# Performance work log

Measured on AMD Instinct MI355X. Metric: run time of the kernel, lower is better.

The kernel has to match this reference:

```python
import jax, jax.numpy as jnp
import numpy as np

NEG_SLOPE = 0.2
EPS = 1e-16


def add_self_loops(edge_index, num_nodes):
    loops = jnp.arange(num_nodes, dtype=edge_index.dtype)
    return jnp.concatenate([edge_index, jnp.stack([loops, loops])], axis=1)


def gat_conv(x, edge_index, W, att_src, att_dst, bias, concat):
    # PyG GATConv: linear -> per-head attention logits -> segment softmax over
    # incoming edges of each destination node -> weighted scatter-add.
    N = x.shape[0]
    H, C = att_src.shape
    ei = add_self_loops(edge_index, N)
    src, dst = ei[0], ei[1]
    h = (x @ W).reshape(N, H, C)                      # [N,H,C]
    a_src = jnp.einsum('nhc,hc->nh', h, att_src)       # [N,H]
    a_dst = jnp.einsum('nhc,hc->nh', h, att_dst)       # [N,H]
    logits = jax.nn.leaky_relu(a_src[src] + a_dst[dst], NEG_SLOPE)  # [E,H]
    m = jax.ops.segment_max(logits, dst, num_segments=N)            # [N,H]
    e = jnp.exp(logits - m[dst])
    s = jax.ops.segment_sum(e, dst, num_segments=N)                 # [N,H]
    alpha = e / (s[dst] + EPS)                                      # [E,H]
    out = jax.ops.segment_sum(h[src] * alpha[:, :, None], dst, num_segments=N)  # [N,H,C]
    out = out.reshape(N, H * C) if concat else out.mean(axis=1)
    return out + bias


def setup_inputs() -> dict:
    key = jax.random.key(0)
    ks = jax.random.split(key, 10)
    N, E, F_in, Hd, heads, F_out = 50000, 800000, 128, 32, 4, 64
    return {
        'x': jax.random.normal(ks[0], (N, F_in), jnp.float32),
        'edge_index': jax.random.randint(ks[1], (2, E), 0, N, jnp.int64),
        'W1': jax.random.normal(ks[2], (F_in, heads * Hd), jnp.float32) * 0.1,
        'att_src1': jax.random.normal(ks[3], (heads, Hd), jnp.float32) * 0.1,
        'att_dst1': jax.random.normal(ks[4], (heads, Hd), jnp.float32) * 0.1,
        'bias1': jax.random.normal(ks[5], (heads * Hd,), jnp.float32) * 0.1,
        'W2': jax.random.normal(ks[6], (heads * Hd, heads * F_out), jnp.float32) * 0.1,
        'att_src2': jax.random.normal(ks[7], (heads, F_out), jnp.float32) * 0.1,
        'att_dst2': jax.random.normal(ks[8], (heads, F_out), jnp.float32) * 0.1,
        'bias2': jax.random.normal(ks[9], (F_out,), jnp.float32) * 0.1,
    }


def reference(x, edge_index, W1, att_src1, att_dst1, bias1, W2, att_src2, att_dst2, bias2):
    h = gat_conv(x, edge_index, W1, att_src1, att_dst1, bias1, concat=True)
    h = jax.nn.elu(h)  # dropout p=0.0 / eval mode -> identity
    out = gat_conv(h, edge_index, W2, att_src2, att_dst2, bias2, concat=False)
    return out
```

## Files before the change

kernel.cpp:

```cpp
#include <hip/hip_runtime.h>

typedef unsigned int uint;
typedef unsigned short ushort;


__device__ __forceinline__ float leaky(float x) { return x >= 0.f ? x : 0.2f * x; }
__device__ __forceinline__ float b2f(ushort h) { return __uint_as_float(((uint)h) << 16); }
__device__ __forceinline__ ushort f2b(float f) {
    uint u = __float_as_uint(f);
    return (ushort)((u + 0x7FFF + ((u >> 16) & 1)) >> 16);
}

#if defined(__has_builtin)
#if __has_builtin(__builtin_amdgcn_fdot2_f32_bf16)
#define HAS_DOT2 1
#endif
#endif
#ifndef HAS_DOT2
#define HAS_DOT2 0
#endif

#if HAS_DOT2
typedef __bf16 bf16v2 __attribute__((ext_vector_type(2)));
__device__ __forceinline__ float dot2bf(uint h2, uint w2, float c) {
    return __builtin_amdgcn_fdot2_f32_bf16(__builtin_bit_cast(bf16v2, h2),
                                           __builtin_bit_cast(bf16v2, w2), c, false);
}
#define DOT2PAIR(hE, hE1, wpk, a0, a1)                                  \
    a0 = dot2bf(__builtin_amdgcn_perm(hE, hE1, 0x01000504), wpk, a0);   \
    a1 = dot2bf(__builtin_amdgcn_perm(hE, hE1, 0x03020706), wpk, a1);
#else
#define DOT2PAIR(hE, hE1, wpk, a0, a1)                                  \
    {                                                                   \
        float wlo = __uint_as_float((wpk) << 16);                       \
        float whi = __uint_as_float((wpk) & 0xffff0000u);               \
        a0 = fmaf(wlo, __uint_as_float((hE) << 16), a0);                \
        a1 = fmaf(wlo, __uint_as_float((hE) & 0xffff0000u), a1);        \
        a0 = fmaf(whi, __uint_as_float((hE1) << 16), a0);               \
        a1 = fmaf(whi, __uint_as_float((hE1) & 0xffff0000u), a1);       \
    }
#endif

__device__ __forceinline__ int detect_bf_local(const void* xin) {
    __shared__ int s_sane;
    if (threadIdx.x == 0) s_sane = 0;
    __syncthreads();
    ushort v = ((const ushort*)xin)[2 * threadIdx.x];
    int ex = (v >> 7) & 0xFF;
    if (v == 0 || (ex >= 100 && ex <= 135)) atomicAdd(&s_sane, 1);
    __syncthreads();
    return s_sane >= 230;
}
__device__ __forceinline__ int detect_is64_local(const int* ei) {
    __shared__ int s_odd;
    if (threadIdx.x == 0) s_odd = 0;
    __syncthreads();
    if (threadIdx.x < 64 && ei[2 * threadIdx.x + 1] != 0) atomicOr(&s_odd, 1);
    __syncthreads();
    return s_odd == 0;
}

__device__ __forceinline__ float rdf(const void* p_, int i, int bf) {
    return bf ? b2f(((const ushort*)p_)[i]) : ((const float*)p_)[i];
}

__device__ __forceinline__ int edge_dst(const int* __restrict__ ei, int E, int e, int is64) {
    return (e >= E) ? (e - E) : (is64 ? ei[2 * E + 2 * e] : ei[E + e]);
}

__global__ void prep_kernel(const void* __restrict__ x, const void* __restrict__ W1,
                            const void* __restrict__ as1, const void* __restrict__ ad1,
                            const void* __restrict__ b1, const void* __restrict__ b2,
                            const void* __restrict__ W2, const void* __restrict__ as2,
                            const void* __restrict__ ad2, const int* __restrict__ ei,
                            int E, int ET,
                            ushort* __restrict__ W1T, float* __restrict__ att1,
                            float* __restrict__ b1f, float* __restrict__ b2f_,
                            float* __restrict__ w2t8, ushort* __restrict__ W2sT,
                            int* __restrict__ flagI, int* __restrict__ flagF,
                            int* __restrict__ bcnt) {
    int b = blockIdx.x, t = threadIdx.x;
    if (b < 64) {
        int bf = detect_bf_local(x);
        int i = b * 256 + t;
        int k = i >> 7, n = i & 127;
        W1T[n * 128 + k] = bf ? ((const ushort*)W1)[i] : f2b(((const float*)W1)[i]);
        return;
    }
    b -= 64;
    if (b == 0) {
        int bf = detect_bf_local(x);
        int is64 = detect_is64_local(ei);
        if (t == 0) { *flagF = bf; *flagI = is64; }
        for (int i = t; i < 512; i += 256) {
            if (i < 128)      att1[i] = rdf(as1, i, bf);
            else if (i < 256) att1[i] = rdf(ad1, i - 128, bf);
            else if (i < 384) b1f[i - 256] = rdf(b1, i - 256, bf);
            else if (i < 448) b2f_[i - 384] = rdf(b2, i - 384, bf);
        }
        return;
    }
    b -= 1;
    if (b < 4) {
        int bf = detect_bf_local(x);
        int idx = b * 256 + t;
        int o = idx >> 7, k = idx & 127, h = o & 3;
        const void* att = (o < 4) ? as2 : ad2;
        float s = 0.f;
        for (int c = 0; c < 64; ++c) s += rdf(W2, k * 256 + h * 64 + c, bf) * rdf(att, h * 64 + c, bf);
        w2t8[o * 128 + k] = s;
        return;
    }
    b -= 4;
    if (b < 128) {
        int bf = detect_bf_local(x);
        int idx = b * 256 + t;
        int c = idx >> 9, hk = idx & 511;
        int h = hk >> 7, k = hk & 127;
        W2sT[c * 512 + hk] = f2b(0.25f * rdf(W2, k * 256 + h * 64 + c, bf));
        return;
    }
    b -= 128;
    {
        int is64 = detect_is64_local(ei);
        __shared__ int bins[256];
        bins[t] = 0;
        __syncthreads();
        int base = b * 4096;
        for (int i = 0; i < 16; ++i) {
            int e = base + i * 256 + t;
            if (e < ET) atomicAdd(&bins[edge_dst(ei, E, e, is64) >> 8], 1);
        }
        __syncthreads();
        if (bins[t]) atomicAdd(&bcnt[t], bins[t]);
    }
}

__global__ __launch_bounds__(256) void bscan_kernel(const int* __restrict__ bcnt,
                                                    int* __restrict__ bbase,
                                                    int* __restrict__ gcur, int NBUK) {
    __shared__ int sc[256];
    int t = threadIdx.x;
    int v = (t < NBUK) ? bcnt[t] : 0;
    sc[t] = v;
    __syncthreads();
    for (int off = 1; off < 256; off <<= 1) {
        int a = (t >= off) ? sc[t - off] : 0;
        __syncthreads();
        sc[t] += a;
        __syncthreads();
    }
    int excl = sc[t] - v;
    if (t < NBUK) { bbase[t] = excl; gcur[t] = excl; }
    if (t == 255) bbase[NBUK] = sc[255];
}

__global__ __launch_bounds__(256) void part_kernel(const int* __restrict__ ei, int E, int ET,
                                                   const int* __restrict__ flagI,
                                                   int* __restrict__ gcur,
                                                   uint* __restrict__ ebuf, int NBUK) {
    __shared__ uint stage[8192];
    __shared__ int cnt_s[256], sc[256], lbase[257], cur[256], gb[256];
    int t = threadIdx.x;
    int base = blockIdx.x * 8192;
    cnt_s[t] = 0;
    __syncthreads();
    int is64 = *flagI;
    uint pk[32];
    short bk[32];
#pragma unroll
    for (int i = 0; i < 32; ++i) {
        int e = base + i * 256 + t;
        if (e < ET) {
            int src, dst;
            if (e >= E) { src = dst = e - E; }
            else if (is64) { src = ei[2 * e]; dst = ei[2 * E + 2 * e]; }
            else           { src = ei[e];     dst = ei[E + e]; }
            pk[i] = (uint)src | ((uint)dst << 16);
            bk[i] = (short)(dst >> 8);
            atomicAdd(&cnt_s[bk[i]], 1);
        } else bk[i] = -1;
    }
    __syncthreads();
    int v = cnt_s[t];
    sc[t] = v;
    __syncthreads();
    for (int off = 1; off < 256; off <<= 1) {
        int a = (t >= off) ? sc[t - off] : 0;
        __syncthreads();
        sc[t] += a;
        __syncthreads();
    }
    lbase[t + 1] = sc[t];
    cur[t] = sc[t] - v;
    if (t == 0) lbase[0] = 0;
    __syncthreads();
#pragma unroll
    for (int i = 0; i < 32; ++i)
        if (bk[i] >= 0) {
            int slot = atomicAdd(&cur[bk[i]], 1);
            stage[slot] = pk[i];
        }
    __syncthreads();
    if (t < NBUK) {
        int c = lbase[t + 1] - lbase[t];
        if (c > 0) gb[t] = atomicAdd(&gcur[t], c);
    }
    __syncthreads();
    int total = lbase[256];
    for (int i = t; i < total; i += 256) {
        int lo = 0, hi = 255;
        while (lo < hi) { int mid = (lo + hi + 1) >> 1; if (lbase[mid] <= i) lo = mid; else hi = mid - 1; }
        ebuf[gb[lo] + (i - lbase[lo])] = stage[i];
    }
}

__global__ __launch_bounds__(256) void bfinal_kernel(const uint* __restrict__ ebuf,
                                                     const int* __restrict__ bbase,
                                                     int* __restrict__ rowptr,
                                                     int* __restrict__ ecol, int N, int NBUK) {
    __shared__ int hist[2048], cur2[2048], ws[4];
    int b = blockIdx.x, t = threadIdx.x;
    int lane = t & 63, wid = t >> 6;
    int d0 = b << 8;
#pragma unroll
    for (int j = 0; j < 8; ++j) hist[t * 8 + j] = 0;
    __syncthreads();
    int s = bbase[b], e2 = bbase[b + 1];
    for (int i = s + t; i < e2; i += 256) {
        uint pk = ebuf[i];
        int key = (((int)(pk >> 16) - d0) << 3) | (int)((pk & 0xffffu) >> 13);
        atomicAdd(&hist[key], 1);
    }
    __syncthreads();
    int loc[8];
    int v = 0;
#pragma unroll
    for (int j = 0; j < 8; ++j) { loc[j] = v; v += hist[t * 8 + j]; }
    int incl = v;
#pragma unroll
    for (int off = 1; off < 64; off <<= 1) {
        int a = __shfl_up(incl, off, 64);
        if (lane >= off) incl += a;
    }
    if (lane == 63) ws[wid] = incl;
    __syncthreads();
    if (t == 0) {
        int acc = 0;
        for (int j = 0; j < 4; ++j) { int x = ws[j]; ws[j] = acc; acc += x; }
    }
    __syncthreads();
    int excl = incl - v + ws[wid];
    int d = d0 + t;
    if (d < N) rowptr[d] = s + excl;
#pragma unroll
    for (int j = 0; j < 8; ++j) cur2[t * 8 + j] = s + excl + loc[j];
    if (b == NBUK - 1 && t == 0) rowptr[N] = bbase[NBUK];
    __syncthreads();
    for (int i = s + t; i < e2; i += 256) {
        uint pk = ebuf[i];
        int key = (((int)(pk >> 16) - d0) << 3) | (int)((pk & 0xffffu) >> 13);
        int pos = atomicAdd(&cur2[key], 1);
        ecol[pos] = (int)(pk & 0xffffu);
    }
}

__global__ void hist_kernel(const int* __restrict__ ei, int E, int N,
                            const int* __restrict__ flag, int* __restrict__ deg) {
    int e = blockIdx.x * blockDim.x + threadIdx.x;
    if (e >= E + N) return;
    atomicAdd(&deg[edge_dst(ei, E, e, *flag)], 1);
}
__global__ void scatter_kernel(const int* __restrict__ ei, int E, int N,
                               const int* __restrict__ flag, const int* __restrict__ rowptr,
                               int* __restrict__ cnt, int* __restrict__ ecol) {
    int e = blockIdx.x * blockDim.x + threadIdx.x;
    if (e >= E + N) return;
    int src, dst;
    if (e >= E) { src = dst = e - E; }
    else if (*flag) { src = ei[2 * e]; dst = ei[2 * E + 2 * e]; }
    else            { src = ei[e];     dst = ei[E + e]; }
    int pos = rowptr[dst] + atomicAdd(&cnt[dst], 1);
    ecol[pos] = src;
}
__global__ __launch_bounds__(1024) void scan1_kernel(const int* __restrict__ deg,
                                                     int* __restrict__ tmp,
                                                     int* __restrict__ bsum, int n) {
    __shared__ int ws[16];
    int tid = threadIdx.x, lane = tid & 63, wid = tid >> 6;
    int i = blockIdx.x * 1024 + tid;
    int v = (i < n) ? deg[i] : 0;
    int incl = v;
#pragma unroll
    for (int off = 1; off < 64; off <<= 1) {
        int t2 = __shfl_up(incl, off, 64);
        if (lane >= off) incl += t2;
    }
    if (lane == 63) ws[wid] = incl;
    __syncthreads();
    if (tid < 16) {
        int wv_ = ws[tid], winc = wv_;
#pragma unroll
        for (int off = 1; off < 16; off <<= 1) {
            int t2 = __shfl_up(winc, off, 16);
            if (tid >= off) winc += t2;
        }
        ws[tid] = winc - wv_;
    }
    __syncthreads();
    int excl = incl - v + ws[wid];
    if (i < n) tmp[i] = excl;
    if (tid == 1023) bsum[blockIdx.x] = excl + v;
}
__global__ void scan2_kernel(int* __restrict__ bsum, int nb) {
    int lane = threadIdx.x;
    int v = (lane < nb) ? bsum[lane] : 0;
    int incl = v;
    for (int off = 1; off < 64; off <<= 1) {
        int t = __shfl_up(incl, off, 64);
        if (lane >= off) incl += t;
    }
    int total = __shfl(incl, nb - 1, 64);
    if (lane < nb) bsum[lane] = incl - v;
    if (lane == 0) bsum[nb] = total;
}
__global__ void scan3_kernel(const int* __restrict__ tmp, const int* __restrict__ bsum,
                             int* __restrict__ rowptr, int* __restrict__ cnt, int n, int nb) {
    int i = blockIdx.x * blockDim.x + threadIdx.x;
    if (i > n) return;
    rowptr[i] = (i == n) ? bsum[nb] : tmp[i] + bsum[i >> 10];
    if (i < n) cnt[i] = 0;
}

typedef __attribute__((ext_vector_type(8))) short bf16x8;
typedef __attribute__((ext_vector_type(4))) float floatx4;

__global__ __launch_bounds__(256) void gemm1_kernel(
    const void* __restrict__ xraw, const int* __restrict__ flagF,
    const ushort* __restrict__ BT, ushort* __restrict__ C,
    const float* __restrict__ att, float4* __restrict__ asrc4, float4* __restrict__ adst4, int M) {
    constexpr int K = 128, NT = 8;
    int lane = threadIdx.x & 63, wv = threadIdx.x >> 6;
    int row0 = (blockIdx.x * 4 + wv) * 16;
    if (row0 >= M) return;
    int m = lane & 15, quad = lane >> 4;
    int rowa = min(row0 + m, M - 1);
    bf16x8 af[4];
    if (*flagF) {
        const bf16x8* arow = (const bf16x8*)((const ushort*)xraw + (size_t)rowa * K);
#pragma unroll
        for (int kk = 0; kk < 4; ++kk) af[kk] = arow[4 * kk + quad];
    } else {
        const float4* arw = (const float4*)((const float*)xraw + (size_t)rowa * K);
#pragma unroll
        for (int kk = 0; kk < 4; ++kk) {
            float4 fa = arw[2 * (4 * kk + quad)];
            float4 fb = arw[2 * (4 * kk + quad) + 1];
            bf16x8 tv;
            tv[0] = (short)f2b(fa.x); tv[1] = (short)f2b(fa.y);
            tv[2] = (short)f2b(fa.z); tv[3] = (short)f2b(fa.w);
            tv[4] = (short)f2b(fb.x); tv[5] = (short)f2b(fb.y);
            tv[6] = (short)f2b(fb.z); tv[7] = (short)f2b(fb.w);
            af[kk] = tv;
        }
    }
    floatx4 acc[NT] = {};
#pragma unroll
    for (int nt = 0; nt < NT; ++nt) {
        const bf16x8* brow = (const bf16x8*)(BT + (size_t)(nt * 16 + m) * K);
#pragma unroll
        for (int kk = 0; kk < 4; ++kk)
            acc[nt] = __builtin_amdgcn_mfma_f32_16x16x32_bf16(af[kk], brow[4 * kk + quad], acc[nt], 0, 0, 0);
    }
#pragma unroll
    for (int nt = 0; nt < NT; ++nt)
#pragma unroll
        for (int r = 0; r < 4; ++r) {
            int row = row0 + quad * 4 + r;
            if (row < M) C[(size_t)row * 128 + nt * 16 + m] = f2b(acc[nt][r]);
        }
    float attS[NT], attD[NT];
#pragma unroll
    for (int nt = 0; nt < NT; ++nt) { attS[nt] = att[nt * 16 + m]; attD[nt] = att[128 + nt * 16 + m]; }
#pragma unroll
    for (int r = 0; r < 4; ++r) {
        float ps[4] = {0, 0, 0, 0}, pd[4] = {0, 0, 0, 0};
#pragma unroll
        for (int nt = 0; nt < NT; ++nt) {
            int h = nt / 2;
            ps[h] = fmaf(acc[nt][r], attS[nt], ps[h]);
            pd[h] = fmaf(acc[nt][r], attD[nt], pd[h]);
        }
#pragma unroll
        for (int off = 1; off < 16; off <<= 1) {
#pragma unroll
            for (int h = 0; h < 4; ++h) {
                ps[h] += __shfl_xor(ps[h], off, 64);
                pd[h] += __shfl_xor(pd[h], off, 64);
            }
        }
        int row = row0 + quad * 4 + r;
        if (m == 0 && row < M) {
            asrc4[row] = make_float4(ps[0], ps[1], ps[2], ps[3]);
            adst4[row] = make_float4(pd[0], pd[1], pd[2], pd[3]);
        }
    }
}

__global__ __launch_bounds__(256) void agg1_kernel(
    const ushort* __restrict__ hsrc, const float4* __restrict__ a_src4,
    const float4* __restrict__ a_dst4, const int* __restrict__ rowptr,
    const int* __restrict__ ecol, const float* __restrict__ bias,
    const float* __restrict__ w2t8, uint4* __restrict__ outz,
    float4* __restrict__ asrc2, float4* __restrict__ adst2, int N) {
    constexpr int SH = 7;
    __shared__ __align__(16) ushort elds[4][4][4][20];
    int lane = threadIdx.x & 63, wv = threadIdx.x >> 6;
    int q = lane >> 4, c = lane & 15, qbase = q << 4;
    int n = blockIdx.x * 16 + wv * 4 + q;
    bool nv = n < N;
    int start = 0, end = 0;
    if (nv) { start = rowptr[n]; end = rowptr[n + 1]; }
    int deg = end - start;
    float4 ad = nv ? a_dst4[n] : make_float4(0.f, 0.f, 0.f, 0.f);
    int hh = c >> 2;
    uint laneoff = (uint)c * 8;
    float acc[8] = {};
    float ss0 = 0.f, ss1 = 0.f, ss2 = 0.f, ss3 = 0.f;

    for (int cs = 0; cs < deg; cs += 16) {
        int len = min(16, deg - cs);
        bool v = c < len;
        int sv = v ? ecol[start + cs + c] : 0;
        float4 as = a_src4[sv];
        float e0 = v ? __expf(fminf(leaky(as.x + ad.x), 60.f)) : 0.f;
        float e1 = v ? __expf(fminf(leaky(as.y + ad.y), 60.f)) : 0.f;
        float e2 = v ? __expf(fminf(leaky(as.z + ad.z), 60.f)) : 0.f;
        float e3 = v ? __expf(fminf(leaky(as.w + ad.w), 60.f)) : 0.f;
        ushort r0 = f2b(e0), r1 = f2b(e1), r2 = f2b(e2), r3 = f2b(e3);
        elds[wv][0][q][c] = r0; elds[wv][1][q][c] = r1;
        elds[wv][2][q][c] = r2; elds[wv][3][q][c] = r3;
        ss0 += b2f(r0); ss1 += b2f(r1); ss2 += b2f(r2); ss3 += b2f(r3);
        for (int e = 0; e < len; e += 4) {
            int s0 = __shfl(sv, qbase + e + 0, 64);
            int s1 = __shfl(sv, qbase + e + 1, 64);
            int s2 = __shfl(sv, qbase + e + 2, 64);
            int s3 = __shfl(sv, qbase + e + 3, 64);
            uint2 w = *(const uint2*)&elds[wv][hh][q][e];
            uint4 h0 = *(const uint4*)(hsrc + (((uint)s0) << SH) + laneoff);
            uint4 h1 = *(const uint4*)(hsrc + (((uint)s1) << SH) + laneoff);
            uint4 h2 = *(const uint4*)(hsrc + (((uint)s2) << SH) + laneoff);
            uint4 h3 = *(const uint4*)(hsrc + (((uint)s3) << SH) + laneoff);
            DOT2PAIR(h0.x, h1.x, w.x, acc[0], acc[1]); DOT2PAIR(h0.y, h1.y, w.x, acc[2], acc[3]);
            DOT2PAIR(h0.z, h1.z, w.x, acc[4], acc[5]); DOT2PAIR(h0.w, h1.w, w.x, acc[6], acc[7]);
            DOT2PAIR(h2.x, h3.x, w.y, acc[0], acc[1]); DOT2PAIR(h2.y, h3.y, w.y, acc[2], acc[3]);
            DOT2PAIR(h2.z, h3.z, w.y, acc[4], acc[5]); DOT2PAIR(h2.w, h3.w, w.y, acc[6], acc[7]);
        }
    }
#pragma unroll
    for (int off = 1; off < 16; off <<= 1) {
        ss0 += __shfl_xor(ss0, off, 64); ss1 += __shfl_xor(ss1, off, 64);
        ss2 += __shfl_xor(ss2, off, 64); ss3 += __shfl_xor(ss3, off, 64);
    }
    if (!nv) return;
    float ih = (hh == 0) ? 1.f / (ss0 + 1e-16f) : (hh == 1) ? 1.f / (ss1 + 1e-16f)
             : (hh == 2) ? 1.f / (ss2 + 1e-16f) : 1.f / (ss3 + 1e-16f);
    float4 bA = ((const float4*)bias)[2 * c], bB = ((const float4*)bias)[2 * c + 1];
    float o[8];
    o[0] = acc[0] * ih + bA.x; o[1] = acc[1] * ih + bA.y;
    o[2] = acc[2] * ih + bA.z; o[3] = acc[3] * ih + bA.w;
    o[4] = acc[4] * ih + bB.x; o[5] = acc[5] * ih + bB.y;
    o[6] = acc[6] * ih + bB.z; o[7] = acc[7] * ih + bB.w;
#pragma unroll
    for (int j = 0; j < 8; ++j) o[j] = o[j] > 0.f ? o[j] : __expf(o[j]) - 1.f;
    uint4 pk;
    pk.x = (uint)f2b(o[0]) | ((uint)f2b(o[1]) << 16);
    pk.y = (uint)f2b(o[2]) | ((uint)f2b(o[3]) << 16);
    pk.z = (uint)f2b(o[4]) | ((uint)f2b(o[5]) << 16);
    pk.w = (uint)f2b(o[6]) | ((uint)f2b(o[7]) << 16);
    outz[(size_t)n * 16 + c] = pk;

    float po[8];
#pragma unroll
    for (int oo = 0; oo < 8; ++oo) {
        float4 wA = ((const float4*)(w2t8 + oo * 128))[2 * c];
        float4 wB = ((const float4*)(w2t8 + oo * 128))[2 * c + 1];
        po[oo] = o[0] * wA.x + o[1] * wA.y + o[2] * wA.z + o[3] * wA.w
               + o[4] * wB.x + o[5] * wB.y + o[6] * wB.z + o[7] * wB.w;
    }
#pragma unroll
    for (int off = 1; off < 16; off <<= 1)
#pragma unroll
        for (int oo = 0; oo < 8; ++oo) po[oo] += __shfl_xor(po[oo], off, 64);
    if (c == 0) {
        asrc2[n] = make_float4(po[0], po[1], po[2], po[3]);
        adst2[n] = make_float4(po[4], po[5], po[6], po[7]);
    }
}

__global__ __launch_bounds__(256) void agg2_kernel(
    const ushort* __restrict__ hsrc, const float4* __restrict__ a_src4,
    const float4* __restrict__ a_dst4, const int* __restrict__ rowptr,
    const int* __restrict__ ecol, const ushort* __restrict__ W2sT,
    const float* __restrict__ b2, float* __restrict__ outp, int N) {
    constexpr int SH = 7;
    __shared__ __align__(16) ushort elds[4][4][4][20];
    __shared__ __align__(16) ushort lds_a[16][520];
    int lane = threadIdx.x & 63, wv = threadIdx.x >> 6;
    int q = lane >> 4, c = lane & 15, qbase = q << 4;
    int n = blockIdx.x * 16 + wv * 4 + q;
    bool nv = n < N;
    int start = 0, end = 0;
    if (nv) { start = rowptr[n]; end = rowptr[n + 1]; }
    int deg = end - start;
    float4 ad = nv ? a_dst4[n] : make_float4(0.f, 0.f, 0.f, 0.f);
    uint laneoff = (uint)c * 8;
    float a0_[8] = {}, a1_[8] = {}, a2_[8] = {}, a3_[8] = {};
    float ss0 = 0.f, ss1 = 0.f, ss2 = 0.f, ss3 = 0.f;

    for (int cs = 0; cs < deg; cs += 16) {
        int len = min(16, deg - cs);
        bool v = c < len;
        int sv = v ? ecol[start + cs + c] : 0;
        float4 as = a_src4[sv];
        float e0 = v ? __expf(fminf(leaky(as.x + ad.x), 60.f)) : 0.f;
        float e1 = v ? __expf(fminf(leaky(as.y + ad.y), 60.f)) : 0.f;
        float e2 = v ? __expf(fminf(leaky(as.z + ad.z), 60.f)) : 0.f;
        float e3 = v ? __expf(fminf(leaky(as.w + ad.w), 60.f)) : 0.f;
        ushort r0 = f2b(e0), r1 = f2b(e1), r2 = f2b(e2), r3 = f2b(e3);
        elds[wv][0][q][c] = r0; elds[wv][1][q][c] = r1;
        elds[wv][2][q][c] = r2; elds[wv][3][q][c] = r3;
        ss0 += b2f(r0); ss1 += b2f(r1); ss2 += b2f(r2); ss3 += b2f(r3);
        for (int e = 0; e < len; e += 4) {
            int s0 = __shfl(sv, qbase + e + 0, 64);
            int s1 = __shfl(sv, qbase + e + 1, 64);
            int s2 = __shfl(sv, qbase + e + 2, 64);
            int s3 = __shfl(sv, qbase + e + 3, 64);
            uint2 w0 = *(const uint2*)&elds[wv][0][q][e];
            uint2 w1 = *(const uint2*)&elds[wv][1][q][e];
            uint2 w2 = *(const uint2*)&elds[wv][2][q][e];
            uint2 w3 = *(const uint2*)&elds[wv][3][q][e];
            uint4 h0 = *(const uint4*)(hsrc + (((uint)s0) << SH) + laneoff);
            uint4 h1 = *(const uint4*)(hsrc + (((uint)s1) << SH) + laneoff);
            uint4 h2 = *(const uint4*)(hsrc + (((uint)s2) << SH) + laneoff);
            uint4 h3 = *(const uint4*)(hsrc + (((uint)s3) << SH) + laneoff);
            DOT2PAIR(h0.x, h1.x, w0.x, a0_[0], a0_[1]); DOT2PAIR(h0.y, h1.y, w0.x, a0_[2], a0_[3]);
            DOT2PAIR(h0.z, h1.z, w0.x, a0_[4], a0_[5]); DOT2PAIR(h0.w, h1.w, w0.x, a0_[6], a0_[7]);
            DOT2PAIR(h0.x, h1.x, w1.x, a1_[0], a1_[1]); DOT2PAIR(h0.y, h1.y, w1.x, a1_[2], a1_[3]);
            DOT2PAIR(h0.z, h1.z, w1.x, a1_[4], a1_[5]); DOT2PAIR(h0.w, h1.w, w1.x, a1_[6], a1_[7]);
            DOT2PAIR(h0.x, h1.x, w2.x, a2_[0], a2_[1]); DOT2PAIR(h0.y, h1.y, w2.x, a2_[2], a2_[3]);
            DOT2PAIR(h0.z, h1.z, w2.x, a2_[4], a2_[5]); DOT2PAIR(h0.w, h1.w, w2.x, a2_[6], a2_[7]);
            DOT2PAIR(h0.x, h1.x, w3.x, a3_[0], a3_[1]); DOT2PAIR(h0.y, h1.y, w3.x, a3_[2], a3_[3]);
            DOT2PAIR(h0.z, h1.z, w3.x, a3_[4], a3_[5]); DOT2PAIR(h0.w, h1.w, w3.x, a3_[6], a3_[7]);
            DOT2PAIR(h2.x, h3.x, w0.y, a0_[0], a0_[1]); DOT2PAIR(h2.y, h3.y, w0.y, a0_[2], a0_[3]);
            DOT2PAIR(h2.z, h3.z, w0.y, a0_[4], a0_[5]); DOT2PAIR(h2.w, h3.w, w0.y, a0_[6], a0_[7]);
            DOT2PAIR(h2.x, h3.x, w1.y, a1_[0], a1_[1]); DOT2PAIR(h2.y, h3.y, w1.y, a1_[2], a1_[3]);
            DOT2PAIR(h2.z, h3.z, w1.y, a1_[4], a1_[5]); DOT2PAIR(h2.w, h3.w, w1.y, a1_[6], a1_[7]);
            DOT2PAIR(h2.x, h3.x, w2.y, a2_[0], a2_[1]); DOT2PAIR(h2.y, h3.y, w2.y, a2_[2], a2_[3]);
            DOT2PAIR(h2.z, h3.z, w2.y, a2_[4], a2_[5]); DOT2PAIR(h2.w, h3.w, w2.y, a2_[6], a2_[7]);
            DOT2PAIR(h2.x, h3.x, w3.y, a3_[0], a3_[1]); DOT2PAIR(h2.y, h3.y, w3.y, a3_[2], a3_[3]);
            DOT2PAIR(h2.z, h3.z, w3.y, a3_[4], a3_[5]); DOT2PAIR(h2.w, h3.w, w3.y, a3_[6], a3_[7]);
        }
    }
#pragma unroll
    for (int off = 1; off < 16; off <<= 1) {
        ss0 += __shfl_xor(ss0, off, 64); ss1 += __shfl_xor(ss1, off, 64);
        ss2 += __shfl_xor(ss2, off, 64); ss3 += __shfl_xor(ss3, off, 64);
    }
    float i0 = 1.f / (ss0 + 1e-16f), i1 = 1.f / (ss1 + 1e-16f);
    float i2 = 1.f / (ss2 + 1e-16f), i3 = 1.f / (ss3 + 1e-16f);
    int slot = wv * 4 + q;
    uint4 pk;
    pk.x = (uint)f2b(a0_[0] * i0) | ((uint)f2b(a0_[1] * i0) << 16);
    pk.y = (uint)f2b(a0_[2] * i0) | ((uint)f2b(a0_[3] * i0) << 16);
    pk.z = (uint)f2b(a0_[4] * i0) | ((uint)f2b(a0_[5] * i0) << 16);
    pk.w = (uint)f2b(a0_[6] * i0) | ((uint)f2b(a0_[7] * i0) << 16);
    *(uint4*)&lds_a[slot][0 * 128 + 8 * c] = pk;
    pk.x = (uint)f2b(a1_[0] * i1) | ((uint)f2b(a1_[1] * i1) << 16);
    pk.y = (uint)f2b(a1_[2] * i1) | ((uint)f2b(a1_[3] * i1) << 16);
    pk.z = (uint)f2b(a1_[4] * i1) | ((uint)f2b(a1_[5] * i1) << 16);
    pk.w = (uint)f2b(a1_[6] * i1) | ((uint)f2b(a1_[7] * i1) << 16);
    *(uint4*)&lds_a[slot][1 * 128 + 8 * c] = pk;
    pk.x = (uint)f2b(a2_[0] * i2) | ((uint)f2b(a2_[1] * i2) << 16);
    pk.y = (uint)f2b(a2_[2] * i2) | ((uint)f2b(a2_[3] * i2) << 16);
    pk.z = (uint)f2b(a2_[4] * i2) | ((uint)f2b(a2_[5] * i2) << 16);
    pk.w = (uint)f2b(a2_[6] * i2) | ((uint)f2b(a2_[7] * i2) << 16);
    *(uint4*)&lds_a[slot][2 * 128 + 8 * c] = pk;
    pk.x = (uint)f2b(a3_[0] * i3) | ((uint)f2b(a3_[1] * i3) << 16);
    pk.y = (uint)f2b(a3_[2] * i3) | ((uint)f2b(a3_[3] * i3) << 16);
    pk.z = (uint)f2b(a3_[4] * i3) | ((uint)f2b(a3_[5] * i3) << 16);
    pk.w = (uint)f2b(a3_[6] * i3) | ((uint)f2b(a3_[7] * i3) << 16);
    *(uint4*)&lds_a[slot][3 * 128 + 8 * c] = pk;
    __syncthreads();

    int m = lane & 15, quad = lane >> 4;
    const bf16x8* arow = (const bf16x8*)&lds_a[m][0];
    const bf16x8* brow = (const bf16x8*)(W2sT + (size_t)(wv * 16 + m) * 512);
    floatx4 acc2 = {};
#pragma unroll
    for (int kk = 0; kk < 16; ++kk)
        acc2 = __builtin_amdgcn_mfma_f32_16x16x32_bf16(arow[4 * kk + quad], brow[4 * kk + quad], acc2, 0, 0, 0);
    float bb = b2[wv * 16 + m];
#pragma unroll
    for (int r = 0; r < 4; ++r) {
        int row = quad * 4 + r;
        int node = blockIdx.x * 16 + row;
        if (node < N) outp[(size_t)node * 64 + wv * 16 + m] = acc2[r] + bb;
    }
}

extern "C" void kernel_launch(void* const* d_in, const int* in_sizes, int n_in,
                              void* d_out, int out_size, void* d_ws, size_t ws_size,
                              hipStream_t stream) {
    const void* x_raw = d_in[0];
    const int*  ei    = (const int*)d_in[1];
    const void* W1_p  = d_in[2];
    const void* as1_p = d_in[3];
    const void* ad1_p = d_in[4];
    const void* b1_p  = d_in[5];
    const void* W2_p  = d_in[6];
    const void* as2_p = d_in[7];
    const void* ad2_p = d_in[8];
    const void* b2_p  = d_in[9];

    const int F_IN = 128;
    const int N = in_sizes[0] / F_IN;
    const int E = in_sizes[1] / 2;
    const int ET = E + N;
    const int NB = (N + 1023) / 1024;
    const int NBUK = (N + 255) >> 8;
    const int NBH = (ET + 4095) / 4096;

    char* p = (char*)d_ws;
    auto alloc = [&](size_t bytes) { char* r = p; p += (bytes + 255) & ~(size_t)255; return r; };
    ushort* W1T   = (ushort*)alloc(128 * 128 * 2);
    ushort* W2sT  = (ushort*)alloc(64 * 512 * 2);
    float*  att1f = (float*)alloc(256 * 4);
    float*  w2t8  = (float*)alloc(8 * 128 * 4);
    float*  b1f   = (float*)alloc(128 * 4);
    float*  b2f   = (float*)alloc(64 * 4);
    ushort* h1    = (ushort*)alloc((size_t)N * 128 * 2);
    ushort* hL1   = (ushort*)alloc((size_t)N * 128 * 2);
    float*  asrc1 = (float*)alloc((size_t)N * 4 * 4);
    float*  adst1 = (float*)alloc((size_t)N * 4 * 4);
    float*  asrc2 = (float*)alloc((size_t)N * 4 * 4);
    float*  adst2 = (float*)alloc((size_t)N * 4 * 4);
    int* deg    = (int*)alloc((size_t)N * 4);
    int* cnt    = (int*)alloc((size_t)N * 4);
    int* tmp    = (int*)alloc((size_t)N * 4);
    int* bsum   = (int*)alloc(128 * 4);
    int* rowptr = (int*)alloc((size_t)(N + 1) * 4);
    int* ecol   = (int*)alloc((size_t)ET * 4);
    uint* ebuf  = (uint*)alloc((size_t)ET * 4);
    int* bcnt   = (int*)alloc(256 * 4);
    int* bbase  = (int*)alloc(257 * 4);
    int* gcur   = (int*)alloc(256 * 4);
    int* flagI  = (int*)alloc(256);
    int* flagF  = (int*)alloc(256);

    hipMemsetAsync(bcnt, 0, 256 * 4, stream);
    prep_kernel<<<64 + 1 + 4 + 128 + NBH, 256, 0, stream>>>(
        x_raw, W1_p, as1_p, ad1_p, b1_p, b2_p, W2_p, as2_p, ad2_p, ei, E, ET,
        W1T, att1f, b1f, b2f, w2t8, W2sT, flagI, flagF, bcnt);

    if (N <= 65536) {
        bscan_kernel<<<1, 256, 0, stream>>>(bcnt, bbase, gcur, NBUK);
        part_kernel<<<(ET + 8191) / 8192, 256, 0, stream>>>(ei, E, ET, flagI, gcur, ebuf, NBUK);
        bfinal_kernel<<<NBUK, 256, 0, stream>>>(ebuf, bbase, rowptr, ecol, N, NBUK);
    } else {
        hipMemsetAsync(deg, 0, (size_t)N * 4, stream);
        int eblocks = (ET + 255) / 256;
        hist_kernel<<<eblocks, 256, 0, stream>>>(ei, E, N, flagI, deg);
        scan1_kernel<<<NB, 1024, 0, stream>>>(deg, tmp, bsum, N);
        scan2_kernel<<<1, 64, 0, stream>>>(bsum, NB);
        scan3_kernel<<<(N + 256) / 256, 256, 0, stream>>>(tmp, bsum, rowptr, cnt, N, NB);
        scatter_kernel<<<eblocks, 256, 0, stream>>>(ei, E, N, flagI, rowptr, cnt, ecol);
    }

    int nblocks16 = (N + 15) / 16;
    int gblocks = (N + 63) / 64;
    gemm1_kernel<<<gblocks, 256, 0, stream>>>(
        x_raw, flagF, W1T, h1, att1f, (float4*)asrc1, (float4*)adst1, N);
    agg1_kernel<<<nblocks16, 256, 0, stream>>>(
        h1, (const float4*)asrc1, (const float4*)adst1, rowptr, ecol, b1f, w2t8,
        (uint4*)hL1, (float4*)asrc2, (float4*)adst2, N);
    agg2_kernel<<<nblocks16, 256, 0, stream>>>(
        hL1, (const float4*)asrc2, (const float4*)adst2, rowptr, ecol, W2sT, b2f,
        (float*)d_out, N);
}
```

Before: 194.6 us.

## Fuse bucket scan into partition kernel and co-launch GEMM1 blocks with partitioning

```diff
diff --git a/kernel.cpp b/kernel.cpp
--- a/kernel.cpp
+++ b/kernel.cpp
@@ -136,31 +136,95 @@
     }
 }
 
-__global__ __launch_bounds__(256) void bscan_kernel(const int* __restrict__ bcnt,
-                                                    int* __restrict__ bbase,
-                                                    int* __restrict__ gcur, int NBUK) {
-    __shared__ int sc[256];
-    int t = threadIdx.x;
-    int v = (t < NBUK) ? bcnt[t] : 0;
-    sc[t] = v;
-    __syncthreads();
-    for (int off = 1; off < 256; off <<= 1) {
-        int a = (t >= off) ? sc[t - off] : 0;
-        __syncthreads();
-        sc[t] += a;
-        __syncthreads();
-    }
-    int excl = sc[t] - v;
-    if (t < NBUK) { bbase[t] = excl; gcur[t] = excl; }
-    if (t == 255) bbase[NBUK] = sc[255];
-}
-
-__global__ __launch_bounds__(256) void part_kernel(const int* __restrict__ ei, int E, int ET,
-                                                   const int* __restrict__ flagI,
-                                                   int* __restrict__ gcur,
-                                                   uint* __restrict__ ebuf, int NBUK) {
+typedef __attribute__((ext_vector_type(8))) short bf16x8;
+typedef __attribute__((ext_vector_type(4))) float floatx4;
+
+__device__ __forceinline__ void gemm1_body(
+    int blk, const void* __restrict__ xraw, const int* __restrict__ flagF,
+    const ushort* __restrict__ BT, ushort* __restrict__ C,
+    const float* __restrict__ att, float4* __restrict__ asrc4, float4* __restrict__ adst4,
+    int M) {
+    constexpr int K = 128, NT = 8;
+    int lane = threadIdx.x & 63, wv = threadIdx.x >> 6;
+    int row0 = (blk * 4 + wv) * 16;
+    if (row0 >= M) return;
+    int m = lane & 15, quad = lane >> 4;
+    int rowa = min(row0 + m, M - 1);
+    bf16x8 af[4];
+    if (*flagF) {
+        const bf16x8* arow = (const bf16x8*)((const ushort*)xraw + (size_t)rowa * K);
+#pragma unroll
+        for (int kk = 0; kk < 4; ++kk) af[kk] = arow[4 * kk + quad];
+    } else {
+        const float4* arw = (const float4*)((const float*)xraw + (size_t)rowa * K);
+#pragma unroll
+        for (int kk = 0; kk < 4; ++kk) {
+            float4 fa = arw[2 * (4 * kk + quad)];
+            float4 fb = arw[2 * (4 * kk + quad) + 1];
+            bf16x8 tv;
+            tv[0] = (short)f2b(fa.x); tv[1] = (short)f2b(fa.y);
+            tv[2] = (short)f2b(fa.z); tv[3] = (short)f2b(fa.w);
+            tv[4] = (short)f2b(fb.x); tv[5] = (short)f2b(fb.y);
+            tv[6] = (short)f2b(fb.z); tv[7] = (short)f2b(fb.w);
+            af[kk] = tv;
+        }
+    }
+    floatx4 acc[NT] = {};
+#pragma unroll
+    for (int nt = 0; nt < NT; ++nt) {
+        const bf16x8* brow = (const bf16x8*)(BT + (size_t)(nt * 16 + m) * K);
+#pragma unroll
+        for (int kk = 0; kk < 4; ++kk)
+            acc[nt] = __builtin_amdgcn_mfma_f32_16x16x32_bf16(af[kk], brow[4 * kk + quad], acc[nt], 0, 0, 0);
+    }
+#pragma unroll
+    for (int nt = 0; nt < NT; ++nt)
+#pragma unroll
+        for (int r = 0; r < 4; ++r) {
+            int row = row0 + quad * 4 + r;
+            if (row < M) C[(size_t)row * 128 + nt * 16 + m] = f2b(acc[nt][r]);
+        }
+    float attS[NT], attD[NT];
+#pragma unroll
+    for (int nt = 0; nt < NT; ++nt) { attS[nt] = att[nt * 16 + m]; attD[nt] = att[128 + nt * 16 + m]; }
+#pragma unroll
+    for (int r = 0; r < 4; ++r) {
+        float ps[4] = {0, 0, 0, 0}, pd[4] = {0, 0, 0, 0};
+#pragma unroll
+        for (int nt = 0; nt < NT; ++nt) {
+            int h = nt / 2;
+            ps[h] = fmaf(acc[nt][r], attS[nt], ps[h]);
+            pd[h] = fmaf(acc[nt][r], attD[nt], pd[h]);
+        }
+#pragma unroll
+        for (int off = 1; off < 16; off <<= 1) {
+#pragma unroll
+            for (int h = 0; h < 4; ++h) {
+                ps[h] += __shfl_xor(ps[h], off, 64);
+                pd[h] += __shfl_xor(pd[h], off, 64);
+            }
+        }
+        int row = row0 + quad * 4 + r;
+        if (m == 0 && row < M) {
+            asrc4[row] = make_float4(ps[0], ps[1], ps[2], ps[3]);
+            adst4[row] = make_float4(pd[0], pd[1], pd[2], pd[3]);
+        }
+    }
+}
+
+__global__ __launch_bounds__(256) void partg_kernel(
+    const int* __restrict__ ei, int E, int ET, const int* __restrict__ flagI,
+    const int* __restrict__ bcnt, int* __restrict__ gofs, uint* __restrict__ ebuf,
+    int NBUK, int npart,
+    const void* __restrict__ xraw, const int* __restrict__ flagF,
+    const ushort* __restrict__ BT, ushort* __restrict__ C, const float* __restrict__ att,
+    float4* __restrict__ asrc4, float4* __restrict__ adst4, int M) {
+    if ((int)blockIdx.x >= npart) {
+        gemm1_body(blockIdx.x - npart, xraw, flagF, BT, C, att, asrc4, adst4, M);
+        return;
+    }
     __shared__ uint stage[8192];
-    __shared__ int cnt_s[256], sc[256], lbase[257], cur[256], gb[256];
+    __shared__ int cnt_s[256], sc[256], sc2[256], lbase[257], cur[256], gb[256];
     int t = threadIdx.x;
     int base = blockIdx.x * 8192;
     cnt_s[t] = 0;
@@ -183,16 +247,20 @@
     }
     __syncthreads();
     int v = cnt_s[t];
+    int v2 = (t < NBUK) ? bcnt[t] : 0;
     sc[t] = v;
+    sc2[t] = v2;
     __syncthreads();
     for (int off = 1; off < 256; off <<= 1) {
-        int a = (t >= off) ? sc[t - off] : 0;
+        int a  = (t >= off) ? sc[t - off]  : 0;
+        int a2 = (t >= off) ? sc2[t - off] : 0;
         __syncthreads();
-        sc[t] += a;
+        sc[t] += a; sc2[t] += a2;
         __syncthreads();
     }
     lbase[t + 1] = sc[t];
     cur[t] = sc[t] - v;
+    int bbx = sc2[t] - v2;
     if (t == 0) lbase[0] = 0;
     __syncthreads();
 #pragma unroll
@@ -204,7 +272,7 @@
     __syncthreads();
     if (t < NBUK) {
         int c = lbase[t + 1] - lbase[t];
-        if (c > 0) gb[t] = atomicAdd(&gcur[t], c);
+        if (c > 0) gb[t] = bbx + atomicAdd(&gofs[t], c);
     }
     __syncthreads();
     int total = lbase[256];
@@ -216,17 +284,26 @@
 }
 
 __global__ __launch_bounds__(256) void bfinal_kernel(const uint* __restrict__ ebuf,
-                                                     const int* __restrict__ bbase,
+                                                     const int* __restrict__ bcnt,
                                                      int* __restrict__ rowptr,
                                                      int* __restrict__ ecol, int N, int NBUK) {
-    __shared__ int hist[2048], cur2[2048], ws[4];
+    __shared__ int hist[2048], cur2[2048], ws[4], bb[256];
     int b = blockIdx.x, t = threadIdx.x;
     int lane = t & 63, wid = t >> 6;
     int d0 = b << 8;
+    bb[t] = (t < NBUK) ? bcnt[t] : 0;
 #pragma unroll
     for (int j = 0; j < 8; ++j) hist[t * 8 + j] = 0;
     __syncthreads();
-    int s = bbase[b], e2 = bbase[b + 1];
+    for (int off = 1; off < 256; off <<= 1) {
+        int a = (t >= off) ? bb[t - off] : 0;
+        __syncthreads();
+        bb[t] += a;
+        __syncthreads();
+    }
+    int s = (b == 0) ? 0 : bb[b - 1];
+    int e2 = bb[b];
+    int total = bb[255];
     for (int i = s + t; i < e2; i += 256) {
         uint pk = ebuf[i];
         int key = (((int)(pk >> 16) - d0) << 3) | (int)((pk & 0xffffu) >> 13);
@@ -255,7 +332,7 @@
     if (d < N) rowptr[d] = s + excl;
 #pragma unroll
     for (int j = 0; j < 8; ++j) cur2[t * 8 + j] = s + excl + loc[j];
-    if (b == NBUK - 1 && t == 0) rowptr[N] = bbase[NBUK];
+    if (b == NBUK - 1 && t == 0) rowptr[N] = total;
     __syncthreads();
     for (int i = s + t; i < e2; i += 256) {
         uint pk = ebuf[i];
@@ -332,79 +409,11 @@
     if (i < n) cnt[i] = 0;
 }
 
-typedef __attribute__((ext_vector_type(8))) short bf16x8;
-typedef __attribute__((ext_vector_type(4))) float floatx4;
-
 __global__ __launch_bounds__(256) void gemm1_kernel(
     const void* __restrict__ xraw, const int* __restrict__ flagF,
     const ushort* __restrict__ BT, ushort* __restrict__ C,
     const float* __restrict__ att, float4* __restrict__ asrc4, float4* __restrict__ adst4, int M) {
-    constexpr int K = 128, NT = 8;
-    int lane = threadIdx.x & 63, wv = threadIdx.x >> 6;
-    int row0 = (blockIdx.x * 4 + wv) * 16;
-    if (row0 >= M) return;
-    int m = lane & 15, quad = lane >> 4;
-    int rowa = min(row0 + m, M - 1);
-    bf16x8 af[4];
-    if (*flagF) {
-        const bf16x8* arow = (const bf16x8*)((const ushort*)xraw + (size_t)rowa * K);
-#pragma unroll
-        for (int kk = 0; kk < 4; ++kk) af[kk] = arow[4 * kk + quad];
-    } else {
-        const float4* arw = (const float4*)((const float*)xraw + (size_t)rowa * K);
-#pragma unroll
-        for (int kk = 0; kk < 4; ++kk) {
-            float4 fa = arw[2 * (4 * kk + quad)];
-            float4 fb = arw[2 * (4 * kk + quad) + 1];
-            bf16x8 tv;
-            tv[0] = (short)f2b(fa.x); tv[1] = (short)f2b(fa.y);
-            tv[2] = (short)f2b(fa.z); tv[3] = (short)f2b(fa.w);
-            tv[4] = (short)f2b(fb.x); tv[5] = (short)f2b(fb.y);
-            tv[6] = (short)f2b(fb.z); tv[7] = (short)f2b(fb.w);
-            af[kk] = tv;
-        }
-    }
-    floatx4 acc[NT] = {};
-#pragma unroll
-    for (int nt = 0; nt < NT; ++nt) {
-        const bf16x8* brow = (const bf16x8*)(BT + (size_t)(nt * 16 + m) * K);
-#pragma unroll
-        for (int kk = 0; kk < 4; ++kk)
-            acc[nt] = __builtin_amdgcn_mfma_f32_16x16x32_bf16(af[kk], brow[4 * kk + quad], acc[nt], 0, 0, 0);
-    }
-#pragma unroll
-    for (int nt = 0; nt < NT; ++nt)
-#pragma unroll
-        for (int r = 0; r < 4; ++r) {
-            int row = row0 + quad * 4 + r;
-            if (row < M) C[(size_t)row * 128 + nt * 16 + m] = f2b(acc[nt][r]);
-        }
-    float attS[NT], attD[NT];
-#pragma unroll
-    for (int nt = 0; nt < NT; ++nt) { attS[nt] = att[nt * 16 + m]; attD[nt] = att[128 + nt * 16 + m]; }
-#pragma unroll
-    for (int r = 0; r < 4; ++r) {
-        float ps[4] = {0, 0, 0, 0}, pd[4] = {0, 0, 0, 0};
-#pragma unroll
-        for (int nt = 0; nt < NT; ++nt) {
-            int h = nt / 2;
-            ps[h] = fmaf(acc[nt][r], attS[nt], ps[h]);
-            pd[h] = fmaf(acc[nt][r], attD[nt], pd[h]);
-        }
-#pragma unroll
-        for (int off = 1; off < 16; off <<= 1) {
-#pragma unroll
-            for (int h = 0; h < 4; ++h) {
-                ps[h] += __shfl_xor(ps[h], off, 64);
-                pd[h] += __shfl_xor(pd[h], off, 64);
-            }
-        }
-        int row = row0 + quad * 4 + r;
-        if (m == 0 && row < M) {
-            asrc4[row] = make_float4(ps[0], ps[1], ps[2], ps[3]);
-            adst4[row] = make_float4(pd[0], pd[1], pd[2], pd[3]);
-        }
-    }
+    gemm1_body(blockIdx.x, xraw, flagF, BT, C, att, asrc4, adst4, M);
 }
 
 __global__ __launch_bounds__(256) void agg1_kernel(
@@ -653,20 +662,22 @@
     int* ecol   = (int*)alloc((size_t)ET * 4);
     uint* ebuf  = (uint*)alloc((size_t)ET * 4);
     int* bcnt   = (int*)alloc(256 * 4);
-    int* bbase  = (int*)alloc(257 * 4);
-    int* gcur   = (int*)alloc(256 * 4);
+    int* gofs   = (int*)alloc(256 * 4);
     int* flagI  = (int*)alloc(256);
     int* flagF  = (int*)alloc(256);
 
-    hipMemsetAsync(bcnt, 0, 256 * 4, stream);
+    hipMemsetAsync(bcnt, 0, 2 * 256 * 4, stream);
     prep_kernel<<<64 + 1 + 4 + 128 + NBH, 256, 0, stream>>>(
         x_raw, W1_p, as1_p, ad1_p, b1_p, b2_p, W2_p, as2_p, ad2_p, ei, E, ET,
         W1T, att1f, b1f, b2f, w2t8, W2sT, flagI, flagF, bcnt);
 
+    int gblocks = (N + 63) / 64;
     if (N <= 65536) {
-        bscan_kernel<<<1, 256, 0, stream>>>(bcnt, bbase, gcur, NBUK);
-        part_kernel<<<(ET + 8191) / 8192, 256, 0, stream>>>(ei, E, ET, flagI, gcur, ebuf, NBUK);
-        bfinal_kernel<<<NBUK, 256, 0, stream>>>(ebuf, bbase, rowptr, ecol, N, NBUK);
+        int npart = (ET + 8191) / 8192;
+        partg_kernel<<<npart + gblocks, 256, 0, stream>>>(
+            ei, E, ET, flagI, bcnt, gofs, ebuf, NBUK, npart,
+            x_raw, flagF, W1T, h1, att1f, (float4*)asrc1, (float4*)adst1, N);
+        bfinal_kernel<<<NBUK, 256, 0, stream>>>(ebuf, bcnt, rowptr, ecol, N, NBUK);
     } else {
         hipMemsetAsync(deg, 0, (size_t)N * 4, stream);
         int eblocks = (ET + 255) / 256;
@@ -675,12 +686,11 @@
         scan2_kernel<<<1, 64, 0, stream>>>(bsum, NB);
         scan3_kernel<<<(N + 256) / 256, 256, 0, stream>>>(tmp, bsum, rowptr, cnt, N, NB);
         scatter_kernel<<<eblocks, 256, 0, stream>>>(ei, E, N, flagI, rowptr, cnt, ecol);
+        gemm1_kernel<<<gblocks, 256, 0, stream>>>(
+            x_raw, flagF, W1T, h1, att1f, (float4*)asrc1, (float4*)adst1, N);
     }
 
     int nblocks16 = (N + 15) / 16;
-    int gblocks = (N + 63) / 64;
-    gemm1_kernel<<<gblocks, 256, 0, stream>>>(
-        x_raw, flagF, W1T, h1, att1f, (float4*)asrc1, (float4*)adst1, N);
     agg1_kernel<<<nblocks16, 256, 0, stream>>>(
         h1, (const float4*)asrc1, (const float4*)adst1, rowptr, ecol, b1f, w2t8,
         (uint4*)hL1, (float4*)asrc2, (float4*)adst2, N);
```

Measured after the change: 179.4 us, median of 2. 7.8% less time.
